# Kernel tuning notes

Hardware: AMD Instinct MI355X
Metric: run time of the kernel (lower is better)

Reference implementation:

```python
import jax, jax.numpy as jnp
import numpy as np

B, L, H = 1, 2048, 2048
D = 4096          # intermediate_size
N = 16            # state_size
R = 128           # time_step_rank
K = 4             # conv_kernel


def setup_inputs() -> dict:
    key = jax.random.key(0)
    ks = jax.random.split(key, 10)
    s = 0.02
    inp = {
        "input_states": jax.random.normal(ks[0], (B, L, H), jnp.float32),
        "W_in": jax.random.normal(ks[1], (H, 2 * D), jnp.float32) * s,
        "conv_kernel": jax.random.normal(ks[2], (D, 1, K), jnp.float32) * 0.5,
        "conv_bias": jnp.zeros((D,), jnp.float32),
        "W_x": jax.random.normal(ks[3], (D, R + 2 * N), jnp.float32) * s,
        "W_dt": jax.random.normal(ks[4], (R, D), jnp.float32) * (R ** -0.5),
        "b_dt": jax.random.normal(ks[5], (D,), jnp.float32) * 0.1 - 4.0,
        "W_out": jax.random.normal(ks[6], (D, H), jnp.float32) * s,
        "A_log": jnp.log(jnp.broadcast_to(jnp.arange(1, N + 1, dtype=jnp.float32)[None, :], (D, N))),
        "D_param": jnp.ones((D,), jnp.float32),
    }
    return inp


def reference(input_states, W_in, conv_kernel, conv_bias, W_x, W_dt, b_dt, W_out, A_log, D_param):
    dtype = input_states.dtype
    # in_proj -> [B, 2D, L]
    proj = jnp.einsum('blh,he->ble', input_states, W_in).transpose(0, 2, 1)
    hidden, gate = jnp.split(proj, 2, axis=1)  # each [B, D, L]

    # depthwise causal conv1d, padding (K-1, K-1) then crop to L (matches module)
    h = jax.lax.conv_general_dilated(
        lhs=hidden, rhs=conv_kernel, window_strides=(1,),
        padding=((K - 1, K - 1),), feature_group_count=D)[..., :L]
    h = h + conv_bias.reshape(1, -1, 1)
    h = jax.nn.silu(h)  # [B, D, L]

    # x_proj on [B, L, D]
    ssm_params = jnp.einsum('bdl,de->ble', h, W_x)  # [B, L, R+2N]
    time_step, Bmat, Cmat = jnp.split(ssm_params, [R, R + N], axis=-1)

    dt = jax.nn.softplus(jnp.einsum('blr,rd->bld', time_step, W_dt) + b_dt)
    dt = dt.transpose(0, 2, 1)  # [B, D, L]

    A = -jnp.exp(A_log.astype(jnp.float32))  # [D, N]
    # discretize: [B, D, L, N]
    dA = jnp.exp(A[None, :, None, :] * dt[..., None])
    dBu = dt[..., None] * Bmat[:, None, :, :].astype(jnp.float32) * h[:, :, :, None].astype(jnp.float32)

    # selective scan over L
    dA_t = dA.transpose(2, 0, 1, 3)    # [L, B, D, N]
    dBu_t = dBu.transpose(2, 0, 1, 3)  # [L, B, D, N]
    C_t = Cmat.transpose(1, 0, 2)      # [L, B, N]

    def step(s, xs):
        a, bu, c = xs
        s = a * s + bu
        y = jnp.einsum('bdn,bn->bd', s.astype(dtype), c)
        return s, y

    s0 = jnp.zeros((B, D, N), jnp.float32)
    _, ys = jax.lax.scan(step, s0, (dA_t, dBu_t, C_t))  # ys [L, B, D]
    y = ys.transpose(1, 2, 0)  # [B, D, L]

    y = y + h * D_param[None, :, None]
    y = y * jax.nn.silu(gate)
    out = jnp.einsum('bdl,dh->blh', y, W_out)  # [B, L, H]
    return out
```

## Files before the change

### kernel.cpp

```cpp
#include <hip/hip_runtime.h>

#define L_DIM 2048
#define H_DIM 2048
#define D_DIM 4096
#define N_ST  16
#define R_TS  128
#define NPAD  256
#define NC    64
#define CL    32
#define KSP   8
#define KSPO  4

typedef unsigned short u16;
typedef short bf16x8 __attribute__((ext_vector_type(8)));
typedef float f32x4 __attribute__((ext_vector_type(4)));

__device__ __forceinline__ u16 f2b(float x) {
  union { float f; unsigned u; } v; v.f = x;
  unsigned r = v.u + 0x7fffu + ((v.u >> 16) & 1u);
  return (u16)(r >> 16);
}
__device__ __forceinline__ float b2f(u16 v) {
  union { unsigned u; float f; } x; x.u = (unsigned)v << 16; return x.f;
}

__device__ __forceinline__ void gl2lds16(const u16* g, u16* l) {
  __builtin_amdgcn_global_load_lds(
      (const __attribute__((address_space(1))) unsigned*)g,
      (__attribute__((address_space(3))) unsigned*)l, 16, 0, 0);
}

#define PREP_NB 30208
__global__ __launch_bounds__(256)
void k_prep(const float* __restrict__ X, u16* __restrict__ Xb,
            const float* __restrict__ W_in, u16* __restrict__ WinT,
            const float* __restrict__ W_x, u16* __restrict__ WxT,
            const float* __restrict__ W_dt, u16* __restrict__ WdtT,
            const float* __restrict__ W_out, u16* __restrict__ WoutT) {
  __shared__ float t[32][33];
  const int b = blockIdx.x;
  if (b < 4096) {
    int i = b * 256 + threadIdx.x;
    float4 v = ((const float4*)X)[i];
    ushort4 o;
    o.x = f2b(v.x); o.y = f2b(v.y); o.z = f2b(v.z); o.w = f2b(v.w);
    ((ushort4*)Xb)[i] = o;
    return;
  }
  const float* src; u16* dst; int R, C, CB, rel;
  if (b < 20480)      { rel = b - 4096;  src = W_in;  dst = WinT;
                        R = H_DIM; C = 2 * D_DIM; CB = (2 * D_DIM) / 32; }
  else if (b < 21504) { rel = b - 20480; src = W_x;   dst = WxT;
                        R = D_DIM; C = R_TS + 2 * N_ST; CB = NPAD / 32; }
  else if (b < 22016) { rel = b - 21504; src = W_dt;  dst = WdtT;
                        R = R_TS;  C = D_DIM; CB = D_DIM / 32; }
  else                { rel = b - 22016; src = W_out; dst = WoutT;
                        R = D_DIM; C = H_DIM; CB = H_DIM / 32; }
  const int x = threadIdx.x & 31, y = threadIdx.x >> 5;
  const int c0 = (rel % CB) * 32, r0 = (rel / CB) * 32;
#pragma unroll
  for (int i = 0; i < 4; ++i) {
    int r = r0 + y + i * 8, c = c0 + x;
    t[y + i * 8][x] = (c < C) ? src[(size_t)r * C + c] : 0.f;
  }
  __syncthreads();
#pragma unroll
  for (int i = 0; i < 4; ++i) {
    int cc = c0 + y + i * 8;
    dst[(size_t)cc * R + r0 + x] = f2b(t[x][y + i * 8]);
  }
}

__global__ __launch_bounds__(512, 2)
void k_gemm256(const u16* __restrict__ A, const u16* __restrict__ Bt,
               u16* __restrict__ C0, u16* __restrict__ C1,
               int M, int N, int K, int NS) {
  __shared__ u16 lA[2][256][64];
  __shared__ u16 lB[2][256][64];
  const int tid = threadIdx.x;
  const int w = tid >> 6, lane = tid & 63;
  const int wm = w >> 2, wn = w & 3;
  const int fr = lane & 15, fq = lane >> 4;
  const int xr = (fr & 7) << 4;
  const int sr = lane >> 3;
  const int sc = ((lane & 7) ^ sr) << 3;
  const int bn = blockIdx.x, bm = blockIdx.y;
  const u16* Ag = A + (size_t)bm * 256 * K;
  const u16* Bg = Bt + (size_t)bn * 256 * K;
  const int NT = K >> 6;

  f32x4 acc[8][4];
#pragma unroll
  for (int i = 0; i < 8; ++i)
#pragma unroll
    for (int j = 0; j < 4; ++j) acc[i][j] = (f32x4){0.f, 0.f, 0.f, 0.f};

  bf16x8 af[4][2];
  bf16x8 bfr[4][2];

#define STAGE_HALF(LT, G, TT, H) do {                                   \
    const int b_ = (TT) & 1; const int kt_ = (TT) << 6;                 \
    const u16* g0_ = (G) + (size_t)((H) * 128 + w * 8 + sr) * K + kt_ + sc; \
    u16* l0_ = &LT[b_][(H) * 128 + w * 8][0];                           \
    gl2lds16(g0_, l0_);                                                 \
    gl2lds16(g0_ + (size_t)64 * K, l0_ + 64 * 64);                      \
  } while (0)

#define LDA_HALF(BB, MH) do {                                           \
    const char* bA_ = (const char*)lA + (size_t)(BB) * 32768;           \
    _Pragma("unroll")                                                   \
    for (int m_ = 0; m_ < 4; ++m_) {                                    \
      const char* rp_ = bA_ + (wm * 128 + (MH) * 64 + m_ * 16 + fr) * 128; \
      af[m_][0] = *(const bf16x8*)(rp_ + ((fq << 4) ^ xr));             \
      af[m_][1] = *(const bf16x8*)(rp_ + ((64 | (fq << 4)) ^ xr));      \
    } } while (0)

#define LDB_HALF(BB, NH) do {                                           \
    const char* bB_ = (const char*)lB + (size_t)(BB) * 32768;           \
    _Pragma("unroll")                                                   \
    for (int n_ = 0; n_ < 2; ++n_) {                                    \
      const char* rp_ = bB_ + (wn * 64 + ((NH) * 2 + n_) * 16 + fr) * 128; \
      bfr[(NH) * 2 + n_][0] = *(const bf16x8*)(rp_ + ((fq << 4) ^ xr)); \
      bfr[(NH) * 2 + n_][1] = *(const bf16x8*)(rp_ + ((64 | (fq << 4)) ^ xr)); \
    } } while (0)

#define MFMA_Q(MH, NH) do {                                             \
    __builtin_amdgcn_s_setprio(1);                                      \
    _Pragma("unroll")                                                   \
    for (int m_ = 0; m_ < 4; ++m_)                                      \
      _Pragma("unroll")                                                 \
      for (int n_ = 0; n_ < 2; ++n_) {                                  \
        acc[(MH)*4+m_][(NH)*2+n_] = __builtin_amdgcn_mfma_f32_16x16x32_bf16( \
            af[m_][0], bfr[(NH)*2+n_][0], acc[(MH)*4+m_][(NH)*2+n_], 0, 0, 0); \
        acc[(MH)*4+m_][(NH)*2+n_] = __builtin_amdgcn_mfma_f32_16x16x32_bf16( \
            af[m_][1], bfr[(NH)*2+n_][1], acc[(MH)*4+m_][(NH)*2+n_], 0, 0, 0); \
      }                                                                 \
    __builtin_amdgcn_s_setprio(0);                                      \
  } while (0)

#define BARF() do { asm volatile("" ::: "memory");                      \
                    __builtin_amdgcn_sched_barrier(0);                  \
                    __builtin_amdgcn_s_barrier();                       \
                    asm volatile("" ::: "memory"); } while (0)

  STAGE_HALF(lA, Ag, 0, 0); STAGE_HALF(lA, Ag, 0, 1);
  STAGE_HALF(lB, Bg, 0, 0); STAGE_HALF(lB, Bg, 0, 1);
  STAGE_HALF(lB, Bg, 1, 0); STAGE_HALF(lB, Bg, 1, 1);
  asm volatile("s_waitcnt vmcnt(4)" ::: "memory");
  BARF();

  for (int t = 0; t < NT; ++t) {
    const int b = t & 1;
    const int ta = (t + 1 == NT) ? 0 : t + 1;
    const int tb = (t + 2 >= NT) ? (t + 2 - NT) : t + 2;
    LDA_HALF(b, 0); LDB_HALF(b, 0);
    STAGE_HALF(lA, Ag, ta, 0);
    MFMA_Q(0, 0);
    BARF();
    LDB_HALF(b, 1);
    STAGE_HALF(lA, Ag, ta, 1);
    MFMA_Q(0, 1);
    BARF();
    LDA_HALF(b, 1);
    STAGE_HALF(lB, Bg, tb, 0);
    MFMA_Q(1, 0);
    BARF();
    STAGE_HALF(lB, Bg, tb, 1);
    MFMA_Q(1, 1);
    asm volatile("s_waitcnt vmcnt(4)" ::: "memory");
    BARF();
  }
  asm volatile("s_waitcnt vmcnt(0)" ::: "memory");

#pragma unroll
  for (int mi = 0; mi < 8; ++mi)
#pragma unroll
    for (int n = 0; n < 4; ++n) {
      int col = bn * 256 + wn * 64 + n * 16 + fr;
      u16* Cd = C0;
      if (col >= NS) { Cd = C1; col -= NS; }
      const int row0 = bm * 256 + wm * 128 + mi * 16 + fq * 4;
#pragma unroll
      for (int j = 0; j < 4; ++j)
        Cd[(size_t)(row0 + j) * NS + col] = f2b(acc[mi][n][j]);
    }
}

__global__ __launch_bounds__(512, 2)
void k_gemm256s(const u16* __restrict__ A, const u16* __restrict__ Bt,
                u16* __restrict__ Cp, int M, int N, int K, int klen) {
  __shared__ u16 lA[2][256][64];
  __shared__ u16 lB[2][256][64];
  const int tid = threadIdx.x;
  const int w = tid >> 6, lane = tid & 63;
  const int wm = w >> 2, wn = w & 3;
  const int fr = lane & 15, fq = lane >> 4;
  const int xr = (fr & 7) << 4;
  const int sr = lane >> 3;
  const int sc = ((lane & 7) ^ sr) << 3;
  const int bn = blockIdx.x, bm = blockIdx.y, z = blockIdx.z;
  const int k0 = z * klen;
  const u16* Ag = A + (size_t)bm * 256 * K;
  const u16* Bg = Bt + (size_t)bn * 256 * K;
  const int NT = klen >> 6;
  u16* C = Cp + (size_t)z * M * N;

  f32x4 acc[8][4];
#pragma unroll
  for (int i = 0; i < 8; ++i)
#pragma unroll
    for (int j = 0; j < 4; ++j) acc[i][j] = (f32x4){0.f, 0.f, 0.f, 0.f};

  bf16x8 af[4][2];
  bf16x8 bfr[4][2];

#undef STAGE_HALF
#define STAGE_HALF(LT, G, TT, H) do {                                   \
    const int b_ = (TT) & 1; const int kt_ = ((TT) << 6) + k0;          \
    const u16* g0_ = (G) + (size_t)((H) * 128 + w * 8 + sr) * K + kt_ + sc; \
    u16* l0_ = &LT[b_][(H) * 128 + w * 8][0];                           \
    gl2lds16(g0_, l0_);                                                 \
    gl2lds16(g0_ + (size_t)64 * K, l0_ + 64 * 64);                      \
  } while (0)

  STAGE_HALF(lA, Ag, 0, 0); STAGE_HALF(lA, Ag, 0, 1);
  STAGE_HALF(lB, Bg, 0, 0); STAGE_HALF(lB, Bg, 0, 1);
  STAGE_HALF(lB, Bg, 1, 0); STAGE_HALF(lB, Bg, 1, 1);
  asm volatile("s_waitcnt vmcnt(4)" ::: "memory");
  BARF();

  for (int t = 0; t < NT; ++t) {
    const int b = t & 1;
    const int ta = (t + 1 == NT) ? 0 : t + 1;
    const int tb = (t + 2 >= NT) ? (t + 2 - NT) : t + 2;
    LDA_HALF(b, 0); LDB_HALF(b, 0);
    STAGE_HALF(lA, Ag, ta, 0);
    MFMA_Q(0, 0);
    BARF();
    LDB_HALF(b, 1);
    STAGE_HALF(lA, Ag, ta, 1);
    MFMA_Q(0, 1);
    BARF();
    LDA_HALF(b, 1);
    STAGE_HALF(lB, Bg, tb, 0);
    MFMA_Q(1, 0);
    BARF();
    STAGE_HALF(lB, Bg, tb, 1);
    MFMA_Q(1, 1);
    asm volatile("s_waitcnt vmcnt(4)" ::: "memory");
    BARF();
  }
  asm volatile("s_waitcnt vmcnt(0)" ::: "memory");

#undef STAGE_HALF
#undef LDA_HALF
#undef LDB_HALF
#undef MFMA_Q
#undef BARF

#pragma unroll
  for (int mi = 0; mi < 8; ++mi)
#pragma unroll
    for (int n = 0; n < 4; ++n) {
      const int col = bn * 256 + wn * 64 + n * 16 + fr;
      const int row0 = bm * 256 + wm * 128 + mi * 16 + fq * 4;
#pragma unroll
      for (int j = 0; j < 4; ++j)
        C[(size_t)(row0 + j) * N + col] = f2b(acc[mi][n][j]);
    }
}

__global__ __launch_bounds__(256)
void k_ored(const u16* __restrict__ Cp, float* __restrict__ out) {
  const int i = blockIdx.x * 256 + threadIdx.x;
  f32x4 s = (f32x4){0.f, 0.f, 0.f, 0.f};
#pragma unroll
  for (int z = 0; z < KSPO; ++z) {
    ushort4 p = *(const ushort4*)&Cp[(size_t)z * L_DIM * H_DIM + (size_t)i * 4];
    s[0] += b2f(p.x); s[1] += b2f(p.y); s[2] += b2f(p.z); s[3] += b2f(p.w);
  }
  *(f32x4*)&out[(size_t)i * 4] = s;
}

__global__ __launch_bounds__(256)
void k_gemm_bt(const u16* __restrict__ A, const u16* __restrict__ Bt,
               float* __restrict__ C, int M, int N, int K) {
  __shared__ u16 sA[128 * 64];
  __shared__ u16 sB[128 * 64];
  const int tid = threadIdx.x;
  const int wave = tid >> 6, lane = tid & 63;
  const int bn = blockIdx.x, bm = blockIdx.y;
  const int wm = wave >> 1, wn = wave & 1;
  const int fr = lane & 15, fq = lane >> 4;
  const int srow = lane >> 3;
  const int scol = (lane & 7) * 8;

  const u16* Ab = A + (size_t)bm * 128 * K;
  const u16* Bb = Bt + (size_t)bn * 128 * K;

  f32x4 acc[4][4];
#pragma unroll
  for (int i = 0; i < 4; ++i)
#pragma unroll
    for (int j = 0; j < 4; ++j) acc[i][j] = (f32x4){0.f, 0.f, 0.f, 0.f};

  for (int kt = 0; kt < K; kt += 64) {
    __syncthreads();
#pragma unroll
    for (int i = 0; i < 4; ++i) {
      int ci = wave * 4 + i;
      int row = ci * 8 + srow;
      gl2lds16(Ab + (size_t)row * K + kt + scol, &sA[ci * 512]);
      gl2lds16(Bb + (size_t)row * K + kt + scol, &sB[ci * 512]);
    }
    __syncthreads();
#pragma unroll
    for (int kk = 0; kk < 2; ++kk) {
      bf16x8 af[4], bfr[4];
#pragma unroll
      for (int mf = 0; mf < 4; ++mf)
        af[mf] = *(const bf16x8*)&sA[(wm * 64 + mf * 16 + fr) * 64 + kk * 32 + fq * 8];
#pragma unroll
      for (int nf = 0; nf < 4; ++nf)
        bfr[nf] = *(const bf16x8*)&sB[(wn * 64 + nf * 16 + fr) * 64 + kk * 32 + fq * 8];
#pragma unroll
      for (int mf = 0; mf < 4; ++mf)
#pragma unroll
        for (int nf = 0; nf < 4; ++nf)
          acc[mf][nf] = __builtin_amdgcn_mfma_f32_16x16x32_bf16(
              af[mf], bfr[nf], acc[mf][nf], 0, 0, 0);
    }
  }

#pragma unroll
  for (int mf = 0; mf < 4; ++mf)
#pragma unroll
    for (int nf = 0; nf < 4; ++nf) {
      int col = bn * 128 + wn * 64 + nf * 16 + fr;
#pragma unroll
      for (int j = 0; j < 4; ++j) {
        int row = bm * 128 + wm * 64 + mf * 16 + fq * 4 + j;
        C[(size_t)row * N + col] = acc[mf][nf][j];
      }
    }
}

__global__ __launch_bounds__(256)
void k_gemm_bt_split(const u16* __restrict__ A, const u16* __restrict__ Bt,
                     float* __restrict__ Cp, int M, int N, int K, int klen) {
  __shared__ u16 sA[128 * 64];
  __shared__ u16 sB[128 * 64];
  const int tid = threadIdx.x;
  const int wave = tid >> 6, lane = tid & 63;
  const int bn = blockIdx.x, bm = blockIdx.y, z = blockIdx.z;
  const int wm = wave >> 1, wn = wave & 1;
  const int fr = lane & 15, fq = lane >> 4;
  const int srow = lane >> 3;
  const int scol = (lane & 7) * 8;
  const int k0 = z * klen;
  float* C = Cp + (size_t)z * M * N;

  const u16* Ab = A + (size_t)bm * 128 * K;
  const u16* Bb = Bt + (size_t)bn * 128 * K;

  f32x4 acc[4][4];
#pragma unroll
  for (int i = 0; i < 4; ++i)
#pragma unroll
    for (int j = 0; j < 4; ++j) acc[i][j] = (f32x4){0.f, 0.f, 0.f, 0.f};

  for (int kt = k0; kt < k0 + klen; kt += 64) {
    __syncthreads();
#pragma unroll
    for (int i = 0; i < 4; ++i) {
      int ci = wave * 4 + i;
      int row = ci * 8 + srow;
      gl2lds16(Ab + (size_t)row * K + kt + scol, &sA[ci * 512]);
      gl2lds16(Bb + (size_t)row * K + kt + scol, &sB[ci * 512]);
    }
    __syncthreads();
#pragma unroll
    for (int kk = 0; kk < 2; ++kk) {
      bf16x8 af[4], bfr[4];
#pragma unroll
      for (int mf = 0; mf < 4; ++mf)
        af[mf] = *(const bf16x8*)&sA[(wm * 64 + mf * 16 + fr) * 64 + kk * 32 + fq * 8];
#pragma unroll
      for (int nf = 0; nf < 4; ++nf)
        bfr[nf] = *(const bf16x8*)&sB[(wn * 64 + nf * 16 + fr) * 64 + kk * 32 + fq * 8];
#pragma unroll
      for (int mf = 0; mf < 4; ++mf)
#pragma unroll
        for (int nf = 0; nf < 4; ++nf)
          acc[mf][nf] = __builtin_amdgcn_mfma_f32_16x16x32_bf16(
              af[mf], bfr[nf], acc[mf][nf], 0, 0, 0);
    }
  }

#pragma unroll
  for (int mf = 0; mf < 4; ++mf)
#pragma unroll
    for (int nf = 0; nf < 4; ++nf) {
      int col = bn * 128 + wn * 64 + nf * 16 + fr;
#pragma unroll
      for (int j = 0; j < 4; ++j) {
        int row = bm * 128 + wm * 64 + mf * 16 + fq * 4 + j;
        C[(size_t)row * N + col] = acc[mf][nf][j];
      }
    }
}

__global__ __launch_bounds__(256)
void k_xred(const float* __restrict__ Cp, float* __restrict__ ssm,
            u16* __restrict__ tsb) {
  int i = blockIdx.x * 256 + threadIdx.x;
  int l = i >> 6, g = i & 63;
  f32x4 s = (f32x4){0.f, 0.f, 0.f, 0.f};
#pragma unroll
  for (int z = 0; z < KSP; ++z)
    s += *(const f32x4*)&Cp[(size_t)z * L_DIM * NPAD + (size_t)l * NPAD + g * 4];
  *(f32x4*)&ssm[(size_t)l * NPAD + g * 4] = s;
  if (g < 32) {
    ushort4 o;
    o.x = f2b(s[0]); o.y = f2b(s[1]); o.z = f2b(s[2]); o.w = f2b(s[3]);
    *(ushort4*)&tsb[(size_t)l * R_TS + g * 4] = o;
  }
}

__global__ __launch_bounds__(256)
void k_conv_silu(const u16* __restrict__ Phid, const float* __restrict__ ck,
                 const float* __restrict__ cb, u16* __restrict__ hb) {
  int idx = blockIdx.x * 256 + threadIdx.x;
  int l = idx >> 12, d = idx & (D_DIM - 1);
  float acc = cb[d];
#pragma unroll
  for (int k = 0; k < 4; ++k) {
    int ll = l - 3 + k;
    if (ll >= 0) acc = fmaf(b2f(Phid[(size_t)ll * D_DIM + d]), ck[d * 4 + k], acc);
  }
  float sv = acc / (1.f + __expf(-acc));
  hb[idx] = f2b(sv);
}

__global__ __launch_bounds__(256)
void k_scan_partial(const float* __restrict__ dtraw, const float* __restrict__ b_dt,
                    const u16* __restrict__ hb, const float* __restrict__ ssm,
                    const float* __restrict__ A_log, float* __restrict__ sC,
                    float* __restrict__ aP) {
  __shared__ float sBl[CL][16];
  const int c = blockIdx.x >> 4;
  const int d = ((blockIdx.x & 15) << 8) + threadIdx.x;
  const int l0 = c * CL;
  {
    int t = threadIdx.x;
    if (t < CL * 4) {
      int r = t >> 2, j = (t & 3) * 4;
      *(float4*)&sBl[r][j] =
          *(const float4*)&ssm[(size_t)(l0 + r) * NPAD + R_TS + j];
    }
  }
  float Ac[N_ST];
#pragma unroll
  for (int n = 0; n < N_ST; ++n) Ac[n] = -__expf(A_log[d * N_ST + n]);
  const float bdt = b_dt[d];
  float s[N_ST], ap[N_ST];
#pragma unroll
  for (int n = 0; n < N_ST; ++n) { s[n] = 0.f; ap[n] = 1.f; }
  __syncthreads();

  float dtn = dtraw[(size_t)l0 * D_DIM + d];
  float hn = b2f(hb[(size_t)l0 * D_DIM + d]);
  for (int i = 0; i < CL; ++i) {
    const float x = dtn + bdt;
    const float hv = hn;
    const int ip = (i + 1 < CL) ? (i + 1) : i;
    dtn = dtraw[(size_t)(l0 + ip) * D_DIM + d];
    hn = b2f(hb[(size_t)(l0 + ip) * D_DIM + d]);
    const float dt = (x > 20.f) ? x : __logf(1.f + __expf(x));
    const float dth = dt * hv;
#pragma unroll
    for (int n = 0; n < N_ST; ++n) {
      float dA = __expf(Ac[n] * dt);
      s[n] = fmaf(dA, s[n], dth * sBl[i][n]);
      ap[n] *= dA;
    }
  }
  float* so = sC + ((size_t)c * D_DIM + d) * N_ST;
  float* ao = aP + ((size_t)c * D_DIM + d) * N_ST;
#pragma unroll
  for (int n = 0; n < N_ST; ++n) { so[n] = s[n]; ao[n] = ap[n]; }
}

__global__ __launch_bounds__(256)
void k_scan_combine(const float* __restrict__ sC, const float* __restrict__ aP,
                    float* __restrict__ init) {
  const int i = blockIdx.x * 256 + threadIdx.x;
  float s = 0.f;
  for (int c = 0; c < NC; ++c) {
    init[(size_t)c * (D_DIM * N_ST) + i] = s;
    s = fmaf(aP[(size_t)c * (D_DIM * N_ST) + i], s,
             sC[(size_t)c * (D_DIM * N_ST) + i]);
  }
}

__global__ __launch_bounds__(256)
void k_scan_final(const float* __restrict__ dtraw, const float* __restrict__ b_dt,
                  const u16* __restrict__ hb, const float* __restrict__ ssm,
                  const float* __restrict__ A_log, const float* __restrict__ init,
                  const u16* __restrict__ Pgate, const float* __restrict__ Dp,
                  u16* __restrict__ yb) {
  __shared__ float sBC[CL][32];
  const int c = blockIdx.x >> 4;
  const int d = ((blockIdx.x & 15) << 8) + threadIdx.x;
  const int l0 = c * CL;
  {
    int t = threadIdx.x;
    if (t < CL * 8) {
      int r = t >> 3, j = (t & 7) * 4;
      *(float4*)&sBC[r][j] =
          *(const float4*)&ssm[(size_t)(l0 + r) * NPAD + R_TS + j];
    }
  }
  float Ac[N_ST];
#pragma unroll
  for (int n = 0; n < N_ST; ++n) Ac[n] = -__expf(A_log[d * N_ST + n]);
  const float bdt = b_dt[d], dpd = Dp[d];
  float s[N_ST];
  const float* ini = init + ((size_t)c * D_DIM + d) * N_ST;
#pragma unroll
  for (int n = 0; n < N_ST; ++n) s[n] = ini[n];
  __syncthreads();

  float dtn = dtraw[(size_t)l0 * D_DIM + d];
  float hn = b2f(hb[(size_t)l0 * D_DIM + d]);
  float gn = b2f(Pgate[(size_t)l0 * D_DIM + d]);
  for (int i = 0; i < CL; ++i) {
    const float x = dtn + bdt;
    const float hv = hn;
    const float gv = gn;
    const int ip = (i + 1 < CL) ? (i + 1) : i;
    dtn = dtraw[(size_t)(l0 + ip) * D_DIM + d];
    hn = b2f(hb[(size_t)(l0 + ip) * D_DIM + d]);
    gn = b2f(Pgate[(size_t)(l0 + ip) * D_DIM + d]);
    const float dt = (x > 20.f) ? x : __logf(1.f + __expf(x));
    const float dth = dt * hv;
    float y = 0.f;
#pragma unroll
    for (int n = 0; n < N_ST; ++n) {
      float dA = __expf(Ac[n] * dt);
      s[n] = fmaf(dA, s[n], dth * sBC[i][n]);
      y = fmaf(s[n], sBC[i][16 + n], y);
    }
    y = fmaf(hv, dpd, y);
    const float sg = gv / (1.f + __expf(-gv));
    yb[(size_t)(l0 + i) * D_DIM + d] = f2b(y * sg);
  }
}

extern "C" void kernel_launch(void* const* d_in, const int* in_sizes, int n_in,
                              void* d_out, int out_size, void* d_ws, size_t ws_size,
                              hipStream_t stream) {
  const float* X     = (const float*)d_in[0];
  const float* W_in  = (const float*)d_in[1];
  const float* ck    = (const float*)d_in[2];
  const float* cb    = (const float*)d_in[3];
  const float* W_x   = (const float*)d_in[4];
  const float* W_dt  = (const float*)d_in[5];
  const float* b_dt  = (const float*)d_in[6];
  const float* W_out = (const float*)d_in[7];
  const float* A_log = (const float*)d_in[8];
  const float* Dp    = (const float*)d_in[9];

  char* w = (char*)d_ws;
  size_t off = 0;
  auto alloc = [&](size_t bytes) {
    void* p = w + off;
    off = (off + bytes + 255) & ~(size_t)255;
    return p;
  };
  u16*   Xb    = (u16*)  alloc((size_t)L_DIM * H_DIM * 2);
  u16*   WinT  = (u16*)  alloc((size_t)2 * D_DIM * H_DIM * 2);
  u16*   Phid  = (u16*)  alloc((size_t)L_DIM * D_DIM * 2);
  u16*   Pgate = (u16*)  alloc((size_t)L_DIM * D_DIM * 2);
  u16*   hb    = (u16*)  alloc((size_t)L_DIM * D_DIM * 2);
  u16*   WxT   = (u16*)  alloc((size_t)NPAD * D_DIM * 2);
  float* ssm   = (float*)alloc((size_t)L_DIM * NPAD * 4);
  u16*   tsb   = (u16*)  alloc((size_t)L_DIM * R_TS * 2);
  u16*   WdtT  = (u16*)  alloc((size_t)D_DIM * R_TS * 2);
  float* dtraw = (float*)alloc((size_t)L_DIM * D_DIM * 4);
  u16*   WoutT = (u16*)  alloc((size_t)H_DIM * D_DIM * 2);
  u16*   yb    = (u16*)  alloc((size_t)L_DIM * D_DIM * 2);
  float* xpart  = (float*)d_ws;
  float* sCb    = (float*)d_ws;
  float* aPb    = (float*)((char*)d_ws + (size_t)NC * D_DIM * N_ST * 4);
  float* initb  = (float*)Phid;
  u16*   opartb = (u16*)d_ws;
  (void)ws_size;

  k_prep<<<PREP_NB, 256, 0, stream>>>(
      X, Xb, W_in, WinT, W_x, WxT, W_dt, WdtT, W_out, WoutT);
  k_gemm256<<<dim3(2 * D_DIM / 256, L_DIM / 256), 512, 0, stream>>>(
      Xb, WinT, Phid, Pgate, L_DIM, 2 * D_DIM, H_DIM, D_DIM);
  k_conv_silu<<<L_DIM * D_DIM / 256, 256, 0, stream>>>(Phid, ck, cb, hb);
  k_gemm_bt_split<<<dim3(NPAD / 128, L_DIM / 128, KSP), 256, 0, stream>>>(
      hb, WxT, xpart, L_DIM, NPAD, D_DIM, D_DIM / KSP);
  k_xred<<<L_DIM * NPAD / 4 / 256, 256, 0, stream>>>(xpart, ssm, tsb);
  k_gemm_bt<<<dim3(D_DIM / 128, L_DIM / 128), 256, 0, stream>>>(
      tsb, WdtT, dtraw, L_DIM, D_DIM, R_TS);
  k_scan_partial<<<NC * (D_DIM / 256), 256, 0, stream>>>(
      dtraw, b_dt, hb, ssm, A_log, sCb, aPb);
  k_scan_combine<<<D_DIM * N_ST / 256, 256, 0, stream>>>(sCb, aPb, initb);
  k_scan_final<<<NC * (D_DIM / 256), 256, 0, stream>>>(
      dtraw, b_dt, hb, ssm, A_log, initb, Pgate, Dp, yb);
  k_gemm256s<<<dim3(H_DIM / 256, L_DIM / 256, KSPO), 512, 0, stream>>>(
      yb, WoutT, opartb, L_DIM, H_DIM, D_DIM, D_DIM / KSPO);
  k_ored<<<L_DIM * H_DIM / 4 / 256, 256, 0, stream>>>(opartb, (float*)d_out);
}
```

Before: 306.5 us.

## Restructure GEMM main loop into two phases with full fragment loads

Each k-tile now loads all A and B fragments from LDS up front and issues both A-stage halves together, then runs two MFMA halves separated by one barrier instead of four quarter phases with three barriers. The goal is fewer barriers per iteration and fewer LDS-load and MFMA interleaving stalls. The cost is a larger A fragment array (8x2 vectors), which raises register pressure and can reduce occupancy. It also adds an explicit lgkmcnt(0) wait before the mid-loop barrier and reorders the prologue to stage B tile 0 before A.

```diff
diff --git a/kernel.cpp b/kernel.cpp
--- a/kernel.cpp
+++ b/kernel.cpp
@@ -95,7 +95,7 @@
 #pragma unroll
     for (int j = 0; j < 4; ++j) acc[i][j] = (f32x4){0.f, 0.f, 0.f, 0.f};
 
-  bf16x8 af[4][2];
+  bf16x8 af[8][2];
   bf16x8 bfr[4][2];
 
 #define STAGE_HALF(LT, G, TT, H) do {                                   \
@@ -106,34 +106,34 @@
     gl2lds16(g0_ + (size_t)64 * K, l0_ + 64 * 64);                      \
   } while (0)
 
-#define LDA_HALF(BB, MH) do {                                           \
+#define LDA_FULL(BB) do {                                               \
     const char* bA_ = (const char*)lA + (size_t)(BB) * 32768;           \
     _Pragma("unroll")                                                   \
-    for (int m_ = 0; m_ < 4; ++m_) {                                    \
-      const char* rp_ = bA_ + (wm * 128 + (MH) * 64 + m_ * 16 + fr) * 128; \
+    for (int m_ = 0; m_ < 8; ++m_) {                                    \
+      const char* rp_ = bA_ + (wm * 128 + m_ * 16 + fr) * 128;          \
       af[m_][0] = *(const bf16x8*)(rp_ + ((fq << 4) ^ xr));             \
       af[m_][1] = *(const bf16x8*)(rp_ + ((64 | (fq << 4)) ^ xr));      \
     } } while (0)
 
-#define LDB_HALF(BB, NH) do {                                           \
+#define LDB_FULL(BB) do {                                               \
     const char* bB_ = (const char*)lB + (size_t)(BB) * 32768;           \
     _Pragma("unroll")                                                   \
-    for (int n_ = 0; n_ < 2; ++n_) {                                    \
-      const char* rp_ = bB_ + (wn * 64 + ((NH) * 2 + n_) * 16 + fr) * 128; \
-      bfr[(NH) * 2 + n_][0] = *(const bf16x8*)(rp_ + ((fq << 4) ^ xr)); \
-      bfr[(NH) * 2 + n_][1] = *(const bf16x8*)(rp_ + ((64 | (fq << 4)) ^ xr)); \
+    for (int n_ = 0; n_ < 4; ++n_) {                                    \
+      const char* rp_ = bB_ + (wn * 64 + n_ * 16 + fr) * 128;           \
+      bfr[n_][0] = *(const bf16x8*)(rp_ + ((fq << 4) ^ xr));            \
+      bfr[n_][1] = *(const bf16x8*)(rp_ + ((64 | (fq << 4)) ^ xr));     \
     } } while (0)
 
-#define MFMA_Q(MH, NH) do {                                             \
+#define MFMA_H(MH) do {                                                 \
     __builtin_amdgcn_s_setprio(1);                                      \
     _Pragma("unroll")                                                   \
     for (int m_ = 0; m_ < 4; ++m_)                                      \
       _Pragma("unroll")                                                 \
-      for (int n_ = 0; n_ < 2; ++n_) {                                  \
-        acc[(MH)*4+m_][(NH)*2+n_] = __builtin_amdgcn_mfma_f32_16x16x32_bf16( \
-            af[m_][0], bfr[(NH)*2+n_][0], acc[(MH)*4+m_][(NH)*2+n_], 0, 0, 0); \
-        acc[(MH)*4+m_][(NH)*2+n_] = __builtin_amdgcn_mfma_f32_16x16x32_bf16( \
-            af[m_][1], bfr[(NH)*2+n_][1], acc[(MH)*4+m_][(NH)*2+n_], 0, 0, 0); \
+      for (int n_ = 0; n_ < 4; ++n_) {                                  \
+        acc[(MH)*4+m_][n_] = __builtin_amdgcn_mfma_f32_16x16x32_bf16(   \
+            af[(MH)*4+m_][0], bfr[n_][0], acc[(MH)*4+m_][n_], 0, 0, 0); \
+        acc[(MH)*4+m_][n_] = __builtin_amdgcn_mfma_f32_16x16x32_bf16(   \
+            af[(MH)*4+m_][1], bfr[n_][1], acc[(MH)*4+m_][n_], 0, 0, 0); \
       }                                                                 \
     __builtin_amdgcn_s_setprio(0);                                      \
   } while (0)
@@ -142,9 +142,10 @@
                     __builtin_amdgcn_sched_barrier(0);                  \
                     __builtin_amdgcn_s_barrier();                       \
                     asm volatile("" ::: "memory"); } while (0)
-
+#define LGKM0() asm volatile("s_waitcnt lgkmcnt(0)" ::: "memory")
+
+  STAGE_HALF(lB, Bg, 0, 0); STAGE_HALF(lB, Bg, 0, 1);
   STAGE_HALF(lA, Ag, 0, 0); STAGE_HALF(lA, Ag, 0, 1);
-  STAGE_HALF(lB, Bg, 0, 0); STAGE_HALF(lB, Bg, 0, 1);
   STAGE_HALF(lB, Bg, 1, 0); STAGE_HALF(lB, Bg, 1, 1);
   asm volatile("s_waitcnt vmcnt(4)" ::: "memory");
   BARF();
@@ -153,20 +154,13 @@
     const int b = t & 1;
     const int ta = (t + 1 == NT) ? 0 : t + 1;
     const int tb = (t + 2 >= NT) ? (t + 2 - NT) : t + 2;
-    LDA_HALF(b, 0); LDB_HALF(b, 0);
-    STAGE_HALF(lA, Ag, ta, 0);
-    MFMA_Q(0, 0);
+    LDA_FULL(b); LDB_FULL(b);
+    STAGE_HALF(lA, Ag, ta, 0); STAGE_HALF(lA, Ag, ta, 1);
+    MFMA_H(0);
+    LGKM0();
     BARF();
-    LDB_HALF(b, 1);
-    STAGE_HALF(lA, Ag, ta, 1);
-    MFMA_Q(0, 1);
-    BARF();
-    LDA_HALF(b, 1);
-    STAGE_HALF(lB, Bg, tb, 0);
-    MFMA_Q(1, 0);
-    BARF();
-    STAGE_HALF(lB, Bg, tb, 1);
-    MFMA_Q(1, 1);
+    STAGE_HALF(lB, Bg, tb, 0); STAGE_HALF(lB, Bg, tb, 1);
+    MFMA_H(1);
     asm volatile("s_waitcnt vmcnt(4)" ::: "memory");
     BARF();
   }
@@ -211,7 +205,7 @@
 #pragma unroll
     for (int j = 0; j < 4; ++j) acc[i][j] = (f32x4){0.f, 0.f, 0.f, 0.f};
 
-  bf16x8 af[4][2];
+  bf16x8 af[8][2];
   bf16x8 bfr[4][2];
 
 #undef STAGE_HALF
@@ -223,8 +217,8 @@
     gl2lds16(g0_ + (size_t)64 * K, l0_ + 64 * 64);                      \
   } while (0)
 
+  STAGE_HALF(lB, Bg, 0, 0); STAGE_HALF(lB, Bg, 0, 1);
   STAGE_HALF(lA, Ag, 0, 0); STAGE_HALF(lA, Ag, 0, 1);
-  STAGE_HALF(lB, Bg, 0, 0); STAGE_HALF(lB, Bg, 0, 1);
   STAGE_HALF(lB, Bg, 1, 0); STAGE_HALF(lB, Bg, 1, 1);
   asm volatile("s_waitcnt vmcnt(4)" ::: "memory");
   BARF();
@@ -233,30 +227,24 @@
     const int b = t & 1;
     const int ta = (t + 1 == NT) ? 0 : t + 1;
     const int tb = (t + 2 >= NT) ? (t + 2 - NT) : t + 2;
-    LDA_HALF(b, 0); LDB_HALF(b, 0);
-    STAGE_HALF(lA, Ag, ta, 0);
-    MFMA_Q(0, 0);
+    LDA_FULL(b); LDB_FULL(b);
+    STAGE_HALF(lA, Ag, ta, 0); STAGE_HALF(lA, Ag, ta, 1);
+    MFMA_H(0);
+    LGKM0();
     BARF();
-    LDB_HALF(b, 1);
-    STAGE_HALF(lA, Ag, ta, 1);
-    MFMA_Q(0, 1);
-    BARF();
-    LDA_HALF(b, 1);
-    STAGE_HALF(lB, Bg, tb, 0);
-    MFMA_Q(1, 0);
-    BARF();
-    STAGE_HALF(lB, Bg, tb, 1);
-    MFMA_Q(1, 1);
+    STAGE_HALF(lB, Bg, tb, 0); STAGE_HALF(lB, Bg, tb, 1);
+    MFMA_H(1);
     asm volatile("s_waitcnt vmcnt(4)" ::: "memory");
     BARF();
   }
   asm volatile("s_waitcnt vmcnt(0)" ::: "memory");
 
 #undef STAGE_HALF
-#undef LDA_HALF
-#undef LDB_HALF
-#undef MFMA_Q
+#undef LDA_FULL
+#undef LDB_FULL
+#undef MFMA_H
 #undef BARF
+#undef LGKM0
 
 #pragma unroll
   for (int mi = 0; mi < 8; ++mi)
```

After: 307.9 us. About the same (+0.4%).
